# Kernel optimization log

Hardware: AMD Instinct MI355X
Metric: run time of the kernel (lower is better)

## Reference

```python
import jax, jax.numpy as jnp
import numpy as np

N_HEAD = 6


def setup_inputs() -> dict:
    key = jax.random.key(0)
    k1, k2, k3 = jax.random.split(key, 3)
    B, N, D = 16, 512, 768
    d_head = D // N_HEAD
    p_mask = jnp.ones((B, N), dtype=jnp.float32)
    feature = jax.random.normal(k1, (B, N, D), dtype=jnp.float32)
    # nn.Linear weights (out, in); scaled like torch default init
    W = jax.random.normal(k2, (D, D), dtype=jnp.float32) / np.sqrt(D)
    # attn Linear(2*d_head -> n_head); only the diagonal head rows are used
    Wa = jax.random.normal(k3, (N_HEAD, 2 * d_head), dtype=jnp.float32) / np.sqrt(2 * d_head)
    return {"p_mask": p_mask, "feature": feature, "W": W, "Wa": Wa, "num_layers": 2}


def reference(p_mask, feature, W, Wa, num_layers):
    B, N, D = feature.shape
    H = N_HEAD
    Dh = D // H
    # adj[b,q,k] = p_mask[b,q] * p_mask[b,k]  (bmm of unsqueezed mask)
    adj = p_mask[:, :, None] * p_mask[:, None, :]  # (B,N,N)
    mask = adj[:, :, :, None] > 0                   # (B,N,N,1)
    for _ in range(num_layers):
        residual = feature
        qk = (feature @ W.T).reshape(B, N, H, Dh)  # (B,N,H,Dh)
        # concat(q,k) @ Wa[h] decomposes into query part + key part
        sq = jnp.einsum('bqhd,hd->bqh', qk, Wa[:, :Dh])
        sk = jnp.einsum('bkhd,hd->bkh', qk, Wa[:, Dh:])
        score = jnp.tanh(sq[:, :, None, :] + sk[:, None, :, :])  # (B,N,N,H)
        # masked_fill with -1e-8 where adj == 0 (faithful to source)
        score = jnp.where(mask, score, jnp.float32(-1e-8))
        attn = jax.nn.softmax(score, axis=2)  # softmax over key dim (dim=-2)
        # dropout p=0 in eval -> identity
        hid = jnp.tanh(jnp.einsum('bqkh,bkhd->bqhd', attn, qk))  # (B,N,H,Dh)
        feature = residual + hid.reshape(B, N, D)
    return feature
```

## Files before the change

kernel.cpp:

```cpp
#include <hip/hip_runtime.h>
#include <hip/hip_bf16.h>
#include <stdint.h>

#define BATCH 16
#define NSEQ  512
#define DMODEL 768
#define NHEAD 6
#define DHEAD 128
#define MROWS (BATCH * NSEQ)
#define QBLK  16
#define KTILE 64

typedef __attribute__((ext_vector_type(8))) __bf16 bf16x8;
typedef __attribute__((ext_vector_type(4))) __bf16 bf16x4;
typedef __attribute__((ext_vector_type(4))) float  f32x4;
typedef __attribute__((ext_vector_type(4))) unsigned int u32x4;

#define GLD16(gp, lp) __builtin_amdgcn_global_load_lds( \
    (const __attribute__((address_space(1))) unsigned int*)(gp), \
    (__attribute__((address_space(3))) unsigned int*)(lp), 16, 0, 0)

#define BAR_PLAIN() do { asm volatile("" ::: "memory"); \
    __builtin_amdgcn_s_barrier(); asm volatile("" ::: "memory"); } while (0)
#define BAR_LGKM() do { asm volatile("s_waitcnt lgkmcnt(0)" ::: "memory"); \
    __builtin_amdgcn_s_barrier(); asm volatile("" ::: "memory"); } while (0)

__global__ void cvt_bf16_kernel(const float* __restrict__ src,
                                __bf16* __restrict__ dst, int n4) {
    int i = blockIdx.x * blockDim.x + threadIdx.x;
    if (i < n4) {
        float4 v = reinterpret_cast<const float4*>(src)[i];
        bf16x4 o;
        o.x = (__bf16)v.x; o.y = (__bf16)v.y; o.z = (__bf16)v.z; o.w = (__bf16)v.w;
        reinterpret_cast<bf16x4*>(dst)[i] = o;
    }
}

__global__ __launch_bounds__(256) void gemm_bt(const __bf16* __restrict__ A,
                                               const __bf16* __restrict__ Bm,
                                               __bf16* __restrict__ C,
                                               const float* __restrict__ Wa,
                                               const float* __restrict__ pmask,
                                               float* __restrict__ eq_t,
                                               float* __restrict__ ek_t) {
    __shared__ __align__(16) __bf16 As[2][64 * 32];
    __shared__ __align__(16) __bf16 Bs[2][128 * 32];
    const int tid  = threadIdx.x;
    const int lane = tid & 63;
    const int wave = tid >> 6;
    const int wm = wave >> 1, wn = wave & 1;

    const int wg  = blockIdx.x;
    const int nid = (wg & 7) * 96 + (wg >> 3);
    const int bx  = nid % 6;
    const int by  = nid / 6;
    const int m0 = by * 64;
    const int n0 = bx * 128;

    f32x4 acc[2][4] = {};

    const int e0   = tid * 8;
    const int row0 = tid >> 2;
    const int k0i  = (tid & 3) * 8;

    const int lr = lane & 15;
    const int lg = lane >> 4;
    const int kb = lg * 8;

    #define STAGE(kt, bufi) do { \
        GLD16(A  + (size_t)(m0 + row0)      * DMODEL + (kt) + k0i, &As[bufi][e0]); \
        GLD16(Bm + (size_t)(n0 + row0)      * DMODEL + (kt) + k0i, &Bs[bufi][e0]); \
        GLD16(Bm + (size_t)(n0 + row0 + 64) * DMODEL + (kt) + k0i, &Bs[bufi][e0 + 2048]); \
    } while (0)

    STAGE(0, 0);

    for (int t = 0; t < 24; t++) {
        const int buf = t & 1;
        if (t < 23) {
            STAGE((t + 1) * 32, buf ^ 1);
            asm volatile("s_waitcnt vmcnt(3)" ::: "memory");
        } else {
            asm volatile("s_waitcnt vmcnt(0)" ::: "memory");
        }
        __builtin_amdgcn_s_barrier();
        asm volatile("" ::: "memory");

        bf16x8 af[2], bfv[4];
        #pragma unroll
        for (int i = 0; i < 2; i++)
            af[i] = *reinterpret_cast<const bf16x8*>(&As[buf][(wm * 32 + i * 16 + lr) * 32 + kb]);
        #pragma unroll
        for (int j = 0; j < 4; j++)
            bfv[j] = *reinterpret_cast<const bf16x8*>(&Bs[buf][(wn * 64 + j * 16 + lr) * 32 + kb]);
        #pragma unroll
        for (int i = 0; i < 2; i++)
            #pragma unroll
            for (int j = 0; j < 4; j++)
                acc[i][j] = __builtin_amdgcn_mfma_f32_16x16x32_bf16(af[i], bfv[j], acc[i][j], 0, 0, 0);

        BAR_PLAIN();
    }
    #undef STAGE

    const int rg = lg * 4;
    #pragma unroll
    for (int i = 0; i < 2; i++) {
        #pragma unroll
        for (int j = 0; j < 4; j++) {
            #pragma unroll
            for (int r = 0; r < 4; r++) {
                int row = m0 + wm * 32 + i * 16 + rg + r;
                int col = n0 + wn * 64 + j * 16 + lr;
                C[(size_t)row * DMODEL + col] = (__bf16)acc[i][j][r];
            }
        }
    }

    const int h = bx;
    float wqv[4], wkv[4];
    #pragma unroll
    for (int j = 0; j < 4; j++) {
        int d = wn * 64 + j * 16 + lr;
        wqv[j] = Wa[h * 256 + d];
        wkv[j] = Wa[h * 256 + 128 + d];
    }
    float* red = reinterpret_cast<float*>(&As[0][0]);
    #pragma unroll
    for (int i = 0; i < 2; i++) {
        #pragma unroll
        for (int r = 0; r < 4; r++) {
            float aq = 0.f, ak = 0.f;
            #pragma unroll
            for (int j = 0; j < 4; j++) {
                aq += acc[i][j][r] * wqv[j];
                ak += acc[i][j][r] * wkv[j];
            }
            #pragma unroll
            for (int off = 1; off < 16; off <<= 1) {
                aq += __shfl_xor(aq, off);
                ak += __shfl_xor(ak, off);
            }
            if (lr == 0) {
                int row = wm * 32 + i * 16 + rg + r;
                red[(0 * 64 + row) * 2 + wn] = aq;
                red[(1 * 64 + row) * 2 + wn] = ak;
            }
        }
    }
    __syncthreads();
    if (tid < 64) {
        int row = m0 + tid;
        float s = red[tid * 2] + red[tid * 2 + 1];
        eq_t[(size_t)h * MROWS + row] = (pmask[row] > 0.f) ? __expf(2.f * s) : 0.f;
    } else if (tid < 128) {
        int rl  = tid - 64;
        int row = m0 + rl;
        float s = red[(64 + rl) * 2] + red[(64 + rl) * 2 + 1];
        ek_t[(size_t)h * MROWS + row] = (pmask[row] > 0.f) ? __expf(2.f * s) : 0.f;
    }
}

__global__ __launch_bounds__(256) void attn_pv(const __bf16* __restrict__ QK,
                                               const float* __restrict__ eq_t,
                                               const float* __restrict__ ek_t,
                                               const float* __restrict__ residual,
                                               float* __restrict__ out,
                                               __bf16* __restrict__ out_bf) {
    const int wg  = blockIdx.x;
    const int nid = (wg & 7) * 384 + (wg >> 3);
    const int qt = nid & 31;
    const int hb = nid >> 5;
    const int h  = hb % NHEAD;
    const int b  = hb / NHEAD;
    const int q0 = qt * QBLK;

    __shared__ __align__(16) __bf16 w[QBLK][512];
    __shared__ __align__(16) __bf16 Vt[DHEAD * KTILE];
    const int tid  = threadIdx.x;
    const int lane = tid & 63;
    const int wave = tid >> 6;

    const int wd0 = wave * 32;
    const int lr  = lane & 15;
    const int lg  = lane >> 4;

    const int sd0 = (tid & 15) * 8;
    const int sk0 = (tid >> 4) * 4;
    const __bf16* Vbase = QK + (size_t)b * NSEQ * DMODEL + (size_t)h * DHEAD + sd0;
    char* vtb = reinterpret_cast<char*>(&Vt[0]);

    u32x4 A0, A1, A2, A3, B0, B1, B2, B3;
    #define LOADS(S0, S1, S2, S3, t) do { \
        const __bf16* p = Vbase + (size_t)((t) * KTILE + sk0) * DMODEL; \
        S0 = *reinterpret_cast<const u32x4*>(p); \
        S1 = *reinterpret_cast<const u32x4*>(p + DMODEL); \
        S2 = *reinterpret_cast<const u32x4*>(p + 2 * DMODEL); \
        S3 = *reinterpret_cast<const u32x4*>(p + 3 * DMODEL); \
    } while (0)
    #define WRITEV(S0, S1, S2, S3) do { \
        _Pragma("unroll") \
        for (int j = 0; j < 8; j++) { \
            int d = sd0 + j; \
            int swz = j ^ (tid & 7); \
            unsigned sel = (j & 1) ? 0x07060302u : 0x05040100u; \
            unsigned lo = __builtin_amdgcn_perm(S1[j >> 1], S0[j >> 1], sel); \
            unsigned hi = __builtin_amdgcn_perm(S3[j >> 1], S2[j >> 1], sel); \
            unsigned long long pk = (unsigned long long)lo | ((unsigned long long)hi << 32); \
            *reinterpret_cast<unsigned long long*>(vtb + d * 128 + ((sk0 ^ (swz << 3)) * 2)) = pk; \
        } \
    } while (0)

    LOADS(A0, A1, A2, A3, 0);
    LOADS(B0, B1, B2, B3, 1);

    float res[4][2];
    #pragma unroll
    for (int r = 0; r < 4; r++) {
        int ql = lg * 4 + r;
        #pragma unroll
        for (int n = 0; n < 2; n++) {
            int d = wd0 + n * 16 + lr;
            res[r][n] = residual[((size_t)(b * NSEQ + q0 + ql)) * DMODEL + (size_t)h * DHEAD + d];
        }
    }

    const int k0 = lane * 8;
    const size_t sbase = (size_t)h * MROWS + b * NSEQ;
    float4 e0v = *reinterpret_cast<const float4*>(&ek_t[sbase + k0]);
    float4 e1v = *reinterpret_cast<const float4*>(&ek_t[sbase + k0 + 4]);
    float ek[8] = {e0v.x, e0v.y, e0v.z, e0v.w, e1v.x, e1v.y, e1v.z, e1v.w};
    float eq[4];
    #pragma unroll
    for (int g = 0; g < 4; g++)
        eq[g] = eq_t[sbase + q0 + wave * 4 + g];

    WRITEV(A0, A1, A2, A3);
    LOADS(A0, A1, A2, A3, 2);

    #pragma unroll
    for (int g = 0; g < 4; g++) {
        int q = wave * 4 + g;
        float eqv = eq[g];
        bf16x8 wv;
        #pragma unroll
        for (int j = 0; j < 8; j++) {
            float u = eqv * ek[j];
            float z = __builtin_amdgcn_rcpf(u + 1.f);
            float p = __expf(fmaf(z, -2.f, 1.f));
            wv[j] = (__bf16)(u > 0.f ? p : 1.0f);
        }
        *reinterpret_cast<bf16x8*>(&w[q][k0 ^ ((q & 7) << 3)]) = wv;
    }
    BAR_LGKM();

    bf16x8 vones;
    #pragma unroll
    for (int e = 0; e < 8; e++) vones[e] = (__bf16)1.0f;

    f32x4 acc[2] = {};
    f32x4 accs = {};

    const int wswz = (lr & 7) << 3;

    #pragma unroll
    for (int t = 0; t < 8; t++) {
        __builtin_amdgcn_s_setprio(1);
        #pragma unroll
        for (int ks = 0; ks < 2; ks++) {
            bf16x8 af = *reinterpret_cast<const bf16x8*>(&w[lr][(t * 64 + ks * 32 + lg * 8) ^ wswz]);
            #pragma unroll
            for (int n = 0; n < 2; n++) {
                int d    = wd0 + n * 16 + lr;
                int kbk  = ks * 4 + lg;
                int swzd = (d & 7) ^ ((d >> 3) & 7);
                bf16x8 bv = *reinterpret_cast<const bf16x8*>(vtb + d * 128 + ((kbk ^ swzd) << 4));
                acc[n] = __builtin_amdgcn_mfma_f32_16x16x32_bf16(af, bv, acc[n], 0, 0, 0);
            }
            accs = __builtin_amdgcn_mfma_f32_16x16x32_bf16(af, vones, accs, 0, 0, 0);
        }
        __builtin_amdgcn_s_setprio(0);
        BAR_PLAIN();
        if (t < 7) {
            if ((t & 1) == 0) WRITEV(B0, B1, B2, B3);
            else              WRITEV(A0, A1, A2, A3);
        }
        if (t < 5) {
            if ((t & 1) == 0) LOADS(B0, B1, B2, B3, t + 3);
            else              LOADS(A0, A1, A2, A3, t + 3);
        }
        BAR_LGKM();
    }

    #pragma unroll
    for (int r = 0; r < 4; r++) {
        int ql = lg * 4 + r;
        float rden = __builtin_amdgcn_rcpf(accs[r]);
        #pragma unroll
        for (int n = 0; n < 2; n++) {
            int d  = wd0 + n * 16 + lr;
            float hv = acc[n][r] * rden;
            float e2 = __expf(2.f * hv);
            float tv = 1.f - 2.f * __builtin_amdgcn_rcpf(e2 + 1.f);
            size_t o = ((size_t)(b * NSEQ + q0 + ql)) * DMODEL + (size_t)h * DHEAD + d;
            float ov = res[r][n] + tv;
            out[o] = ov;
            if (out_bf) out_bf[o] = (__bf16)ov;
        }
    }
    #undef LOADS
    #undef WRITEV
}

extern "C" void kernel_launch(void* const* d_in, const int* in_sizes, int n_in,
                              void* d_out, int out_size, void* d_ws, size_t ws_size,
                              hipStream_t stream) {
    const float* pmask   = (const float*)d_in[0];
    const float* feature = (const float*)d_in[1];
    const float* W       = (const float*)d_in[2];
    const float* Wa      = (const float*)d_in[3];
    float* out = (float*)d_out;
    char* ws = (char*)d_ws;

    __bf16* Abf  = (__bf16*)ws;
    __bf16* Wbf  = (__bf16*)(ws + 12582912);
    __bf16* QKbf = (__bf16*)(ws + 12582912 + 1179648);
    float*  eq   = (float*)(ws + 12582912 + 1179648 + 12582912);
    float*  ek   = eq + MROWS * NHEAD;

    const int featN4 = (MROWS * DMODEL) / 4;
    const int wN4    = (DMODEL * DMODEL) / 4;

    hipLaunchKernelGGL(cvt_bf16_kernel, dim3((wN4 + 255) / 256), dim3(256), 0, stream,
                       W, Wbf, wN4);

    hipLaunchKernelGGL(cvt_bf16_kernel, dim3((featN4 + 255) / 256), dim3(256), 0, stream,
                       feature, Abf, featN4);
    hipLaunchKernelGGL(gemm_bt, dim3(768), dim3(256), 0, stream,
                       Abf, Wbf, QKbf, Wa, pmask, eq, ek);
    hipLaunchKernelGGL(attn_pv, dim3(3072), dim3(256), 0, stream,
                       QKbf, eq, ek, feature, out, Abf);

    hipLaunchKernelGGL(gemm_bt, dim3(768), dim3(256), 0, stream,
                       Abf, Wbf, QKbf, Wa, pmask, eq, ek);
    hipLaunchKernelGGL(attn_pv, dim3(3072), dim3(256), 0, stream,
                       QKbf, eq, ek, out, out, (__bf16*)nullptr);
}
```

Before: 119.6 us.

## Double query block per workgroup and double-buffer V tiles in attention kernel

Each attention workgroup now handles 32 query rows instead of 16, so every V tile loaded and transposed into shared memory feeds twice as many MFMAs, and the grid is halved. The V tile buffer is double-buffered so the next tile is written while the current one is consumed, leaving one barrier per iteration instead of two. In exchange, each workgroup uses more shared memory and registers and there are fewer workgroups to fill the GPU.

```diff
diff --git a/kernel.cpp b/kernel.cpp
--- a/kernel.cpp
+++ b/kernel.cpp
@@ -8,7 +8,7 @@
 #define NHEAD 6
 #define DHEAD 128
 #define MROWS (BATCH * NSEQ)
-#define QBLK  16
+#define QBLK  32
 #define KTILE 64
 
 typedef __attribute__((ext_vector_type(8))) __bf16 bf16x8;
@@ -168,15 +168,15 @@
                                                float* __restrict__ out,
                                                __bf16* __restrict__ out_bf) {
     const int wg  = blockIdx.x;
-    const int nid = (wg & 7) * 384 + (wg >> 3);
-    const int qt = nid & 31;
-    const int hb = nid >> 5;
+    const int nid = (wg & 7) * 192 + (wg >> 3);
+    const int qt = nid & 15;
+    const int hb = nid >> 4;
     const int h  = hb % NHEAD;
     const int b  = hb / NHEAD;
     const int q0 = qt * QBLK;
 
     __shared__ __align__(16) __bf16 w[QBLK][512];
-    __shared__ __align__(16) __bf16 Vt[DHEAD * KTILE];
+    __shared__ __align__(16) __bf16 Vt[2][DHEAD * KTILE];
     const int tid  = threadIdx.x;
     const int lane = tid & 63;
     const int wave = tid >> 6;
@@ -188,7 +188,6 @@
     const int sd0 = (tid & 15) * 8;
     const int sk0 = (tid >> 4) * 4;
     const __bf16* Vbase = QK + (size_t)b * NSEQ * DMODEL + (size_t)h * DHEAD + sd0;
-    char* vtb = reinterpret_cast<char*>(&Vt[0]);
 
     u32x4 A0, A1, A2, A3, B0, B1, B2, B3;
     #define LOADS(S0, S1, S2, S3, t) do { \
@@ -198,7 +197,8 @@
         S2 = *reinterpret_cast<const u32x4*>(p + 2 * DMODEL); \
         S3 = *reinterpret_cast<const u32x4*>(p + 3 * DMODEL); \
     } while (0)
-    #define WRITEV(S0, S1, S2, S3) do { \
+    #define WRITEV(S0, S1, S2, S3, bufi) do { \
+        char* vtw = reinterpret_cast<char*>(&Vt[bufi][0]); \
         _Pragma("unroll") \
         for (int j = 0; j < 8; j++) { \
             int d = sd0 + j; \
@@ -207,21 +207,24 @@
             unsigned lo = __builtin_amdgcn_perm(S1[j >> 1], S0[j >> 1], sel); \
             unsigned hi = __builtin_amdgcn_perm(S3[j >> 1], S2[j >> 1], sel); \
             unsigned long long pk = (unsigned long long)lo | ((unsigned long long)hi << 32); \
-            *reinterpret_cast<unsigned long long*>(vtb + d * 128 + ((sk0 ^ (swz << 3)) * 2)) = pk; \
+            *reinterpret_cast<unsigned long long*>(vtw + d * 128 + ((sk0 ^ (swz << 3)) * 2)) = pk; \
         } \
     } while (0)
 
     LOADS(A0, A1, A2, A3, 0);
     LOADS(B0, B1, B2, B3, 1);
 
-    float res[4][2];
-    #pragma unroll
-    for (int r = 0; r < 4; r++) {
-        int ql = lg * 4 + r;
-        #pragma unroll
-        for (int n = 0; n < 2; n++) {
-            int d = wd0 + n * 16 + lr;
-            res[r][n] = residual[((size_t)(b * NSEQ + q0 + ql)) * DMODEL + (size_t)h * DHEAD + d];
+    float res[2][4][2];
+    #pragma unroll
+    for (int qh = 0; qh < 2; qh++) {
+        #pragma unroll
+        for (int r = 0; r < 4; r++) {
+            int ql = qh * 16 + lg * 4 + r;
+            #pragma unroll
+            for (int n = 0; n < 2; n++) {
+                int d = wd0 + n * 16 + lr;
+                res[qh][r][n] = residual[((size_t)(b * NSEQ + q0 + ql)) * DMODEL + (size_t)h * DHEAD + d];
+            }
         }
     }
 
@@ -230,17 +233,17 @@
     float4 e0v = *reinterpret_cast<const float4*>(&ek_t[sbase + k0]);
     float4 e1v = *reinterpret_cast<const float4*>(&ek_t[sbase + k0 + 4]);
     float ek[8] = {e0v.x, e0v.y, e0v.z, e0v.w, e1v.x, e1v.y, e1v.z, e1v.w};
-    float eq[4];
-    #pragma unroll
-    for (int g = 0; g < 4; g++)
-        eq[g] = eq_t[sbase + q0 + wave * 4 + g];
-
-    WRITEV(A0, A1, A2, A3);
+    float eq[8];
+    #pragma unroll
+    for (int g = 0; g < 8; g++)
+        eq[g] = eq_t[sbase + q0 + wave * 8 + g];
+
+    WRITEV(A0, A1, A2, A3, 0);
     LOADS(A0, A1, A2, A3, 2);
 
     #pragma unroll
-    for (int g = 0; g < 4; g++) {
-        int q = wave * 4 + g;
+    for (int g = 0; g < 8; g++) {
+        int q = wave * 8 + g;
         float eqv = eq[g];
         bf16x8 wv;
         #pragma unroll
@@ -258,54 +261,62 @@
     #pragma unroll
     for (int e = 0; e < 8; e++) vones[e] = (__bf16)1.0f;
 
-    f32x4 acc[2] = {};
-    f32x4 accs = {};
+    f32x4 acc[2][2] = {};
+    f32x4 accs[2] = {};
 
     const int wswz = (lr & 7) << 3;
 
     #pragma unroll
     for (int t = 0; t < 8; t++) {
+        const int buf = t & 1;
+        const char* vtr = reinterpret_cast<const char*>(&Vt[buf][0]);
+        if (t < 7) {
+            if ((t & 1) == 0) WRITEV(B0, B1, B2, B3, buf ^ 1);
+            else              WRITEV(A0, A1, A2, A3, buf ^ 1);
+        }
+        if (t < 5) {
+            if ((t & 1) == 0) LOADS(B0, B1, B2, B3, t + 3);
+            else              LOADS(A0, A1, A2, A3, t + 3);
+        }
         __builtin_amdgcn_s_setprio(1);
         #pragma unroll
         for (int ks = 0; ks < 2; ks++) {
-            bf16x8 af = *reinterpret_cast<const bf16x8*>(&w[lr][(t * 64 + ks * 32 + lg * 8) ^ wswz]);
+            int cb = (t * 64 + ks * 32 + lg * 8) ^ wswz;
+            bf16x8 af0 = *reinterpret_cast<const bf16x8*>(&w[lr][cb]);
+            bf16x8 af1 = *reinterpret_cast<const bf16x8*>(&w[16 + lr][cb]);
             #pragma unroll
             for (int n = 0; n < 2; n++) {
                 int d    = wd0 + n * 16 + lr;
                 int kbk  = ks * 4 + lg;
                 int swzd = (d & 7) ^ ((d >> 3) & 7);
-                bf16x8 bv = *reinterpret_cast<const bf16x8*>(vtb + d * 128 + ((kbk ^ swzd) << 4));
-                acc[n] = __builtin_amdgcn_mfma_f32_16x16x32_bf16(af, bv, acc[n], 0, 0, 0);
-            }
-            accs = __builtin_amdgcn_mfma_f32_16x16x32_bf16(af, vones, accs, 0, 0, 0);
+                bf16x8 bv = *reinterpret_cast<const bf16x8*>(vtr + d * 128 + ((kbk ^ swzd) << 4));
+                acc[0][n] = __builtin_amdgcn_mfma_f32_16x16x32_bf16(af0, bv, acc[0][n], 0, 0, 0);
+                acc[1][n] = __builtin_amdgcn_mfma_f32_16x16x32_bf16(af1, bv, acc[1][n], 0, 0, 0);
+            }
+            accs[0] = __builtin_amdgcn_mfma_f32_16x16x32_bf16(af0, vones, accs[0], 0, 0, 0);
+            accs[1] = __builtin_amdgcn_mfma_f32_16x16x32_bf16(af1, vones, accs[1], 0, 0, 0);
         }
         __builtin_amdgcn_s_setprio(0);
-        BAR_PLAIN();
-        if (t < 7) {
-            if ((t & 1) == 0) WRITEV(B0, B1, B2, B3);
-            else              WRITEV(A0, A1, A2, A3);
-        }
-        if (t < 5) {
-            if ((t & 1) == 0) LOADS(B0, B1, B2, B3, t + 3);
-            else              LOADS(A0, A1, A2, A3, t + 3);
-        }
-        BAR_LGKM();
-    }
-
-    #pragma unroll
-    for (int r = 0; r < 4; r++) {
-        int ql = lg * 4 + r;
-        float rden = __builtin_amdgcn_rcpf(accs[r]);
-        #pragma unroll
-        for (int n = 0; n < 2; n++) {
-            int d  = wd0 + n * 16 + lr;
-            float hv = acc[n][r] * rden;
-            float e2 = __expf(2.f * hv);
-            float tv = 1.f - 2.f * __builtin_amdgcn_rcpf(e2 + 1.f);
-            size_t o = ((size_t)(b * NSEQ + q0 + ql)) * DMODEL + (size_t)h * DHEAD + d;
-            float ov = res[r][n] + tv;
-            out[o] = ov;
-            if (out_bf) out_bf[o] = (__bf16)ov;
+        if (t < 7) BAR_LGKM();
+    }
+
+    #pragma unroll
+    for (int qh = 0; qh < 2; qh++) {
+        #pragma unroll
+        for (int r = 0; r < 4; r++) {
+            int ql = qh * 16 + lg * 4 + r;
+            float rden = __builtin_amdgcn_rcpf(accs[qh][r]);
+            #pragma unroll
+            for (int n = 0; n < 2; n++) {
+                int d  = wd0 + n * 16 + lr;
+                float hv = acc[qh][n][r] * rden;
+                float e2 = __expf(2.f * hv);
+                float tv = 1.f - 2.f * __builtin_amdgcn_rcpf(e2 + 1.f);
+                size_t o = ((size_t)(b * NSEQ + q0 + ql)) * DMODEL + (size_t)h * DHEAD + d;
+                float ov = res[qh][r][n] + tv;
+                out[o] = ov;
+                if (out_bf) out_bf[o] = (__bf16)ov;
+            }
         }
     }
     #undef LOADS
@@ -338,11 +349,11 @@
                        feature, Abf, featN4);
     hipLaunchKernelGGL(gemm_bt, dim3(768), dim3(256), 0, stream,
                        Abf, Wbf, QKbf, Wa, pmask, eq, ek);
-    hipLaunchKernelGGL(attn_pv, dim3(3072), dim3(256), 0, stream,
+    hipLaunchKernelGGL(attn_pv, dim3(1536), dim3(256), 0, stream,
                        QKbf, eq, ek, feature, out, Abf);
 
     hipLaunchKernelGGL(gemm_bt, dim3(768), dim3(256), 0, stream,
                        Abf, Wbf, QKbf, Wa, pmask, eq, ek);
-    hipLaunchKernelGGL(attn_pv, dim3(3072), dim3(256), 0, stream,
+    hipLaunchKernelGGL(attn_pv, dim3(1536), dim3(256), 0, stream,
                        QKbf, eq, ek, out, out, (__bf16*)nullptr);
 }
```

After: 110.4 us. -7.7%, faster.
